# Performance work log

Measured on AMD Instinct MI355X. Metric: run time of the kernel, lower is better.

## Reference

```python
import jax, jax.numpy as jnp
import numpy as np
from jax import lax

B, CIN, HC, D, H, W = 4, 16, 16, 31, 128, 128


def setup_inputs() -> dict:
    key = jax.random.key(0)
    k1, k2, k3, k4, k5 = jax.random.split(key, 5)
    inputs = jax.random.normal(k1, (B, CIN, D, H, W), dtype=jnp.float32)
    # Conv3d weight: [out=2*HC, in=CIN, 3,3,3]
    conv_w = jax.random.normal(k2, (2 * HC, CIN, 3, 3, 3), dtype=jnp.float32) * 0.05
    # FFN weights stored as [in, out] (equivalent to torch Linear weight.T)
    w1 = jax.random.normal(k3, (HC, 2 * HC), dtype=jnp.float32) * 0.1
    w2 = jax.random.normal(k4, (2 * HC, HC), dtype=jnp.float32) * 0.1
    w3 = jax.random.normal(k5, (HC, 2 * HC), dtype=jnp.float32) * 0.1
    return {"inputs": inputs, "conv_w": conv_w, "w1": w1, "w2": w2, "w3": w3,
            "reverse": 0}


def reference(inputs, conv_w, w1, w2, w3, reverse):
    hc = conv_w.shape[0] // 2
    # 3D conv producing 2*hc gate channels  [B, 2hc, D, H, W]
    gates = lax.conv_general_dilated(
        inputs, conv_w, window_strides=(1, 1, 1), padding='SAME',
        dimension_numbers=('NCDHW', 'OIDHW', 'NCDHW'))
    Z = jnp.tanh(gates[:, :hc])            # [B, hc, D, H, W]
    F = jax.nn.sigmoid(gates[:, hc:])
    # scan over depth (spectral) dim; h0 = 0 reproduces h = (1-f)*z at step 0
    Zs = jnp.moveaxis(Z, 2, 0)             # [D, B, hc, H, W]
    Fs = jnp.moveaxis(F, 2, 0)
    if reverse:
        Zs, Fs = Zs[::-1], Fs[::-1]

    def step(h, zf):
        z, f = zf
        h = f * h + (1.0 - f) * z
        return h, h

    h0 = jnp.zeros_like(Zs[0])
    _, hs = lax.scan(step, h0, (Zs, Fs))   # [D, B, hc, H, W]
    if reverse:
        hs = hs[::-1]
    out = jnp.moveaxis(hs, 0, 2)           # [B, hc, D, H, W]
    # channel-enhanced FFN on channel-last layout
    x = jnp.moveaxis(out, 1, -1)           # [B, D, H, W, hc]
    x1 = jnp.dot(jax.nn.gelu(jnp.dot(x, w1), approximate=False), w2)
    g = jnp.dot(x, w3)                     # [B, D, H, W, 2hc]
    a, wg = jnp.split(g, 2, axis=-1)
    y = x1 + a * jax.nn.sigmoid(wg)
    return jnp.moveaxis(y, -1, 1)          # [B, hc, D, H, W]
```

## Files before the change

kernel.cpp:

```cpp
#include <hip/hip_runtime.h>
#include <hip/hip_fp16.h>

#define HC 16
#define CIN 16
#define BD 31
#define HH 128
#define WW 128
#define PLANE (HH*WW)
#define CH_STRIDE (BD*PLANE)

typedef __attribute__((ext_vector_type(8))) short bf16x8;
typedef __attribute__((ext_vector_type(16))) float f32x16;

__device__ __forceinline__ float sigmoid_fast(float x) {
    return __builtin_amdgcn_rcpf(1.0f + __expf(-x));
}
__device__ __forceinline__ float tanh_fast(float x) {
    return fmaf(2.0f, __builtin_amdgcn_rcpf(1.0f + __expf(-2.0f * x)), -1.0f);
}
__device__ __forceinline__ ushort f2bf(float f) {
    unsigned u = __float_as_uint(f);
    u = (u + 0x7fffu + ((u >> 16) & 1u)) >> 16;
    return (ushort)u;
}
__device__ __forceinline__ unsigned pack_bf2(float lo, float hi) {
    unsigned r;
    asm("v_cvt_pk_bf16_f32 %0, %1, %2" : "=v"(r) : "v"(lo), "v"(hi));
    return r;
}
__device__ __forceinline__ float gelu_as(float s) {
    float z  = 0.70710678118f * s;
    float az = fabsf(z);
    float t  = __builtin_amdgcn_rcpf(fmaf(0.3275911f, az, 1.0f));
    float p  = t * (0.254829592f + t * (-0.284496736f + t * (1.421413741f
             + t * (-1.453152027f + t * 1.061405429f))));
    float e  = __expf(-z * z);
    float er = copysignf(1.0f - p * e, z);
    return 0.5f * s * (1.0f + er);
}

__global__ void wprep_all(const float* __restrict__ cw,
                          const float* __restrict__ w1,
                          const float* __restrict__ w2,
                          const float* __restrict__ w3,
                          ushort* __restrict__ wtab,
                          ushort* __restrict__ wtab2)
{
    int idx = blockIdx.x * 256 + threadIdx.x;
    if (idx < 13824) {
        int j    = idx & 7;
        int lane = (idx >> 3) & 63;
        int t    = (idx >> 9) % 9;
        int kd   = (idx >> 9) / 9;
        int co = lane & 31;
        int ci = 8 * (lane >> 5) + j;
        int kh = t / 3, kw = t % 3;
        wtab[idx] = f2bf(cw[(co * CIN + ci) * 27 + kd * 9 + kh * 3 + kw]);
        return;
    }
    idx -= 13824;
    if (idx >= 2048) return;
    int e    = idx & 7;
    int lane = (idx >> 3) & 63;
    int tbl  = idx >> 9;
    int m  = lane & 31;
    int hi = lane >> 5;
    int k  = (e & 3) + 8 * (e >> 2) + 4 * hi;
    float v = 0.f;
    if (tbl == 0)      v = w1[k * 32 + m];
    else if (tbl == 3) v = w3[k * 32 + m];
    else {
        int mf = tbl - 1;
        if (m < 16) v = w2[(k + 16 * mf) * 16 + m];
    }
    wtab2[idx] = f2bf(v);
}

__global__ __launch_bounds__(256)
void xprep_kernel(const float* __restrict__ inp, char* __restrict__ xT)
{
    __shared__ float tile[16][256];
    int t  = threadIdx.x;
    int hp = blockIdx.x & 63;
    int g  = blockIdx.x >> 6;
    int d  = g % BD;
    int b  = g / BD;

    size_t src = (size_t)b * CIN * CH_STRIDE + (size_t)d * PLANE + hp * 256;
    #pragma unroll
    for (int c = 0; c < 16; ++c)
        tile[c][t] = inp[src + (size_t)c * CH_STRIDE + t];
    __syncthreads();

    int w  = t & 127;
    int rr = t >> 7;
    char* rowp = xT + (((size_t)(b * BD + d) * 128) + hp * 2 + rr) * 4096;
    #pragma unroll
    for (int q = 0; q < 2; ++q) {
        uint4 pk;
        pk.x = (unsigned)f2bf(tile[q*8+0][t]) | ((unsigned)f2bf(tile[q*8+1][t]) << 16);
        pk.y = (unsigned)f2bf(tile[q*8+2][t]) | ((unsigned)f2bf(tile[q*8+3][t]) << 16);
        pk.z = (unsigned)f2bf(tile[q*8+4][t]) | ((unsigned)f2bf(tile[q*8+5][t]) << 16);
        pk.w = (unsigned)f2bf(tile[q*8+6][t]) | ((unsigned)f2bf(tile[q*8+7][t]) << 16);
        unsigned off = ((unsigned)((w + 1) * 32 + q * 16) ^ (((unsigned)(w + 1) & 0xE) << 3)) - 32;
        *(uint4*)(rowp + off) = pk;
    }
}

#define SLOT_B (3 * 4224)

__device__ __forceinline__ void gload_lds16(const void* g, void* l) {
    __builtin_amdgcn_global_load_lds(
        (const __attribute__((address_space(1))) unsigned int*)g,
        (__attribute__((address_space(3))) unsigned int*)l, 16, 0, 0);
}

__global__ __launch_bounds__(256, 2)
void qrnn_fused(const char* __restrict__ xT,
                const ushort* __restrict__ wtab,
                const ushort* __restrict__ wtab2,
                float* __restrict__ out,
                const int* __restrict__ rev_p)
{
    __shared__ __align__(16) char slab[4][SLOT_B];

    int p = blockIdx.x;
    int logical = (p & 7) * 64 + (p >> 3);
    int b  = logical >> 7;
    int ht = logical & 127;
    int rev = rev_p[0];

    int lane = threadIdx.x & 63;
    int wid  = threadIdx.x >> 6;
    int wl   = lane & 31;
    int hi   = lane >> 5;
    int cio  = hi * 16;

    const bf16x8* wt = (const bf16x8*)wtab;
    bf16x8 af[27];
    #pragma unroll
    for (int t = 0; t < 27; ++t) af[t] = wt[t * 64 + lane];

    const bf16x8* W2 = (const bf16x8*)wtab2;
    bf16x8 af1  = W2[lane];
    bf16x8 af2a = W2[64 + lane];
    bf16x8 af2b = W2[128 + lane];
    bf16x8 af3  = W2[192 + lane];

    unsigned bpo[3];
    #pragma unroll
    for (int dwn = 0; dwn < 3; ++dwn) {
        unsigned wc = (unsigned)(wl + dwn);
        bpo[dwn] = (unsigned)(wid * 1024) + ((wc * 32 + cio) ^ ((wc & 0xE) << 3));
    }

    for (int i = threadIdx.x; i < 4 * 3 * 32; i += 256) {
        int s = i / 96;
        int r = (i / 32) % 3;
        int k = i & 31;
        int off = (k < 8) ? (k * 4) : (4128 + (k - 8) * 4);
        *(int*)(slab[s] + r * 4224 + off) = 0;
    }

    auto zero_slot = [&](int s) {
        for (int i = threadIdx.x; i < 768; i += 256) {
            int r = i >> 8;
            int k = i & 255;
            *(uint4*)(slab[s] + r * 4224 + 32 + k * 16) = uint4{0, 0, 0, 0};
        }
    };

    auto stage = [&](int s, int plane) {
        const char* pl = xT + ((size_t)(b * BD + plane) * 128) * 4096;
        for (int c = wid; c < 12; c += 4) {
            int rr = c >> 2, ch = c & 3;
            int h = ht - 1 + rr;
            char* dst = slab[s] + rr * 4224 + 32 + ch * 1024;
            if ((unsigned)h < (unsigned)HH)
                gload_lds16(pl + (size_t)h * 4096 + ch * 1024 + lane * 16, dst);
            else
                *(uint4*)(dst + lane * 16) = uint4{0, 0, 0, 0};
        }
    };

    f32x16 zacc;
    #pragma unroll
    for (int r = 0; r < 16; ++r) zacc[r] = 0.f;

    auto convd = [&](int d) -> f32x16 {
        f32x16 A = zacc;
        #pragma unroll
        for (int kd = 0; kd < 3; ++kd) {
            const char* sb = slab[(d - 1 + kd) & 3];
            #pragma unroll
            for (int t = 0; t < 9; ++t) {
                bf16x8 bfr = *(const bf16x8*)(sb + (t / 3) * 4224 + bpo[t % 3]);
                A = __builtin_amdgcn_mfma_f32_32x32x16_bf16(af[kd * 9 + t], bfr, A, 0, 0, 0);
            }
        }
        return A;
    };

    float h[8];
    #pragma unroll
    for (int j = 0; j < 8; ++j) h[j] = 0.f;

    float* obase = out + (size_t)b * HC * CH_STRIDE + ht * WW + wid * 32 + wl;

    auto tail = [&](const f32x16& A, int d) {
        union { bf16x8 v; unsigned u[4]; } bx;
        #pragma unroll
        for (int r = 0; r < 8; ++r) {
            float z = tanh_fast(A[r]);
            float f = sigmoid_fast(A[r + 8]);
            h[r] = z + f * (h[r] - z);
        }
        #pragma unroll
        for (int q = 0; q < 4; ++q)
            bx.u[q] = pack_bf2(h[2 * q], h[2 * q + 1]);

        f32x16 a1 = __builtin_amdgcn_mfma_f32_32x32x16_bf16(af1, bx.v, zacc, 0, 0, 0);
        f32x16 a3 = __builtin_amdgcn_mfma_f32_32x32x16_bf16(af3, bx.v, zacc, 0, 0, 0);

        union { bf16x8 v; unsigned u[4]; } b2a, b2b;
        #pragma unroll
        for (int q = 0; q < 4; ++q) {
            b2a.u[q] = pack_bf2(gelu_as(a1[2 * q]),     gelu_as(a1[2 * q + 1]));
            b2b.u[q] = pack_bf2(gelu_as(a1[8 + 2 * q]), gelu_as(a1[8 + 2 * q + 1]));
        }
        f32x16 a2 = __builtin_amdgcn_mfma_f32_32x32x16_bf16(af2a, b2a.v, zacc, 0, 0, 0);
        a2 = __builtin_amdgcn_mfma_f32_32x32x16_bf16(af2b, b2b.v, a2, 0, 0, 0);

        float* ob = obase + (size_t)d * PLANE;
        #pragma unroll
        for (int r = 0; r < 8; ++r) {
            int c = (r & 3) + 8 * (r >> 2) + 4 * hi;
            ob[(size_t)c * CH_STRIDE] = a2[r] + a3[r] * sigmoid_fast(a3[r + 8]);
        }
    };

    int d0  = rev ? (BD - 1) : 0;
    int sgn = rev ? -1 : 1;
    int oobq = rev ? -1 : BD;

    stage(d0 & 3, d0);
    stage((d0 + sgn) & 3, d0 + sgn);
    zero_slot((d0 - sgn) & 3);
    __syncthreads();

    f32x16 accP;
    {
        int q = d0 + 2 * sgn;
        if (q >= 0 && q < BD) stage(q & 3, q);
        accP = convd(d0);
        __syncthreads();
    }

    #pragma unroll 1
    for (int i = 1; i < BD; ++i) {
        int d = d0 + sgn * i;
        int q = d + 2 * sgn;
        if (q >= 0 && q < BD) stage(q & 3, q);
        else if (q == oobq)   zero_slot(q & 3);

        f32x16 acc = convd(d);
        tail(accP, d - sgn);
        accP = acc;

        __syncthreads();
    }
    tail(accP, d0 + sgn * (BD - 1));
}

extern "C" void kernel_launch(void* const* d_in, const int* in_sizes, int n_in,
                              void* d_out, int out_size, void* d_ws, size_t ws_size,
                              hipStream_t stream)
{
    const float* inp = (const float*)d_in[0];
    const float* cw  = (const float*)d_in[1];
    const float* w1  = (const float*)d_in[2];
    const float* w2  = (const float*)d_in[3];
    const float* w3  = (const float*)d_in[4];
    const int*   rev = (const int*)d_in[5];

    ushort* wtab  = (ushort*)d_ws;
    ushort* wtab2 = (ushort*)((char*)d_ws + 27648);
    char*   xT    = (char*)d_ws + 32768;

    wprep_all<<<dim3(62), dim3(256), 0, stream>>>(cw, w1, w2, w3, wtab, wtab2);

    xprep_kernel<<<dim3(7936), dim3(256), 0, stream>>>(inp, xT);

    qrnn_fused<<<dim3(512), dim3(256), 0, stream>>>(
        xT, wtab, wtab2, (float*)d_out, rev);
}
```

Before: 143.0 us.

## Split FFN out of scan kernel into separate MFMA kernel; merge weight prep into xprep

Moves the channel FFN (GELU MLP plus gated branch) out of the serial conv+scan kernel into a new fully parallel MFMA kernel. The scan kernel now writes the bf16 hidden state to a workspace buffer. Weight preparation is folded into the xprep launch as extra blocks, which removes one kernel launch. The aim is to shorten the serial per-depth critical path and cut register pressure in the scan kernel. The cost is an extra round trip through global memory for the hidden state, about 32 MB written and read back, and one more launch. Folding weight prep into xprep assumes the weight tables are ready by the time the scan kernel runs, which stream ordering provides.

```diff
diff --git a/kernel.cpp b/kernel.cpp
--- a/kernel.cpp
+++ b/kernel.cpp
@@ -39,46 +39,46 @@
     return 0.5f * s * (1.0f + er);
 }
 
-__global__ void wprep_all(const float* __restrict__ cw,
-                          const float* __restrict__ w1,
-                          const float* __restrict__ w2,
-                          const float* __restrict__ w3,
-                          ushort* __restrict__ wtab,
-                          ushort* __restrict__ wtab2)
+__global__ __launch_bounds__(256)
+void xprep_kernel(const float* __restrict__ inp, char* __restrict__ xT,
+                  const float* __restrict__ cw,
+                  const float* __restrict__ w1,
+                  const float* __restrict__ w2,
+                  const float* __restrict__ w3,
+                  ushort* __restrict__ wtab, ushort* __restrict__ wtab2)
 {
-    int idx = blockIdx.x * 256 + threadIdx.x;
-    if (idx < 13824) {
-        int j    = idx & 7;
+    if (blockIdx.x >= 7936) {
+        int idx = (blockIdx.x - 7936) * 256 + threadIdx.x;
+        if (idx < 13824) {
+            int j    = idx & 7;
+            int lane = (idx >> 3) & 63;
+            int t    = (idx >> 9) % 9;
+            int kd   = (idx >> 9) / 9;
+            int co = lane & 31;
+            int ci = 8 * (lane >> 5) + j;
+            int kh = t / 3, kw = t % 3;
+            wtab[idx] = f2bf(cw[(co * CIN + ci) * 27 + kd * 9 + kh * 3 + kw]);
+            return;
+        }
+        idx -= 13824;
+        if (idx >= 2048) return;
+        int e    = idx & 7;
         int lane = (idx >> 3) & 63;
-        int t    = (idx >> 9) % 9;
-        int kd   = (idx >> 9) / 9;
-        int co = lane & 31;
-        int ci = 8 * (lane >> 5) + j;
-        int kh = t / 3, kw = t % 3;
-        wtab[idx] = f2bf(cw[(co * CIN + ci) * 27 + kd * 9 + kh * 3 + kw]);
+        int tbl  = idx >> 9;
+        int m  = lane & 31;
+        int hi = lane >> 5;
+        int k  = (e & 3) + 8 * (e >> 2) + 4 * hi;
+        float v = 0.f;
+        if (tbl == 0)      v = w1[k * 32 + m];
+        else if (tbl == 3) v = w3[k * 32 + m];
+        else {
+            int mf = tbl - 1;
+            if (m < 16) v = w2[(k + 16 * mf) * 16 + m];
+        }
+        wtab2[idx] = f2bf(v);
         return;
     }
-    idx -= 13824;
-    if (idx >= 2048) return;
-    int e    = idx & 7;
-    int lane = (idx >> 3) & 63;
-    int tbl  = idx >> 9;
-    int m  = lane & 31;
-    int hi = lane >> 5;
-    int k  = (e & 3) + 8 * (e >> 2) + 4 * hi;
-    float v = 0.f;
-    if (tbl == 0)      v = w1[k * 32 + m];
-    else if (tbl == 3) v = w3[k * 32 + m];
-    else {
-        int mf = tbl - 1;
-        if (m < 16) v = w2[(k + 16 * mf) * 16 + m];
-    }
-    wtab2[idx] = f2bf(v);
-}
-
-__global__ __launch_bounds__(256)
-void xprep_kernel(const float* __restrict__ inp, char* __restrict__ xT)
-{
+
     __shared__ float tile[16][256];
     int t  = threadIdx.x;
     int hp = blockIdx.x & 63;
@@ -116,11 +116,10 @@
 }
 
 __global__ __launch_bounds__(256, 2)
-void qrnn_fused(const char* __restrict__ xT,
-                const ushort* __restrict__ wtab,
-                const ushort* __restrict__ wtab2,
-                float* __restrict__ out,
-                const int* __restrict__ rev_p)
+void qrnn_convscan(const char* __restrict__ xT,
+                   const ushort* __restrict__ wtab,
+                   char* __restrict__ hbuf,
+                   const int* __restrict__ rev_p)
 {
     __shared__ __align__(16) char slab[4][SLOT_B];
 
@@ -140,12 +139,6 @@
     bf16x8 af[27];
     #pragma unroll
     for (int t = 0; t < 27; ++t) af[t] = wt[t * 64 + lane];
-
-    const bf16x8* W2 = (const bf16x8*)wtab2;
-    bf16x8 af1  = W2[lane];
-    bf16x8 af2a = W2[64 + lane];
-    bf16x8 af2b = W2[128 + lane];
-    bf16x8 af3  = W2[192 + lane];
 
     unsigned bpo[3];
     #pragma unroll
@@ -205,10 +198,11 @@
     #pragma unroll
     for (int j = 0; j < 8; ++j) h[j] = 0.f;
 
-    float* obase = out + (size_t)b * HC * CH_STRIDE + ht * WW + wid * 32 + wl;
+    int pix = ht * WW + wid * 32 + wl;
+    char* hb0 = hbuf + ((size_t)b * BD * PLANE + pix) * 32 + hi * 16;
 
     auto tail = [&](const f32x16& A, int d) {
-        union { bf16x8 v; unsigned u[4]; } bx;
+        union { uint4 u4; unsigned u[4]; } bx;
         #pragma unroll
         for (int r = 0; r < 8; ++r) {
             float z = tanh_fast(A[r]);
@@ -218,25 +212,7 @@
         #pragma unroll
         for (int q = 0; q < 4; ++q)
             bx.u[q] = pack_bf2(h[2 * q], h[2 * q + 1]);
-
-        f32x16 a1 = __builtin_amdgcn_mfma_f32_32x32x16_bf16(af1, bx.v, zacc, 0, 0, 0);
-        f32x16 a3 = __builtin_amdgcn_mfma_f32_32x32x16_bf16(af3, bx.v, zacc, 0, 0, 0);
-
-        union { bf16x8 v; unsigned u[4]; } b2a, b2b;
-        #pragma unroll
-        for (int q = 0; q < 4; ++q) {
-            b2a.u[q] = pack_bf2(gelu_as(a1[2 * q]),     gelu_as(a1[2 * q + 1]));
-            b2b.u[q] = pack_bf2(gelu_as(a1[8 + 2 * q]), gelu_as(a1[8 + 2 * q + 1]));
-        }
-        f32x16 a2 = __builtin_amdgcn_mfma_f32_32x32x16_bf16(af2a, b2a.v, zacc, 0, 0, 0);
-        a2 = __builtin_amdgcn_mfma_f32_32x32x16_bf16(af2b, b2b.v, a2, 0, 0, 0);
-
-        float* ob = obase + (size_t)d * PLANE;
-        #pragma unroll
-        for (int r = 0; r < 8; ++r) {
-            int c = (r & 3) + 8 * (r >> 2) + 4 * hi;
-            ob[(size_t)c * CH_STRIDE] = a2[r] + a3[r] * sigmoid_fast(a3[r + 8]);
-        }
+        *(uint4*)(hb0 + (size_t)d * (PLANE * 32)) = bx.u4;
     };
 
     int d0  = rev ? (BD - 1) : 0;
@@ -270,6 +246,57 @@
         __syncthreads();
     }
     tail(accP, d0 + sgn * (BD - 1));
+}
+
+__global__ __launch_bounds__(256)
+void mlp_mfma_kernel(const char* __restrict__ hbuf,
+                     const ushort* __restrict__ wtab2,
+                     float* __restrict__ out)
+{
+    int lane = threadIdx.x & 63;
+    int wid  = threadIdx.x >> 6;
+    int p    = lane & 31;
+    int hi   = lane >> 5;
+
+    size_t tile = (size_t)blockIdx.x * 4 + wid;
+    size_t ptg  = tile * 32 + p;
+
+    const bf16x8* W = (const bf16x8*)wtab2;
+    bf16x8 af1  = W[lane];
+    bf16x8 af2a = W[64 + lane];
+    bf16x8 af2b = W[128 + lane];
+    bf16x8 af3  = W[192 + lane];
+    bf16x8 bx   = *(const bf16x8*)(hbuf + ptg * 32 + hi * 16);
+
+    f32x16 zacc;
+    #pragma unroll
+    for (int r = 0; r < 16; ++r) zacc[r] = 0.f;
+
+    f32x16 a1 = __builtin_amdgcn_mfma_f32_32x32x16_bf16(af1, bx, zacc, 0, 0, 0);
+    f32x16 a3 = __builtin_amdgcn_mfma_f32_32x32x16_bf16(af3, bx, zacc, 0, 0, 0);
+
+    union { bf16x8 v; unsigned u[4]; } b2a, b2b;
+    #pragma unroll
+    for (int q = 0; q < 4; ++q) {
+        b2a.u[q] = pack_bf2(gelu_as(a1[2 * q]),     gelu_as(a1[2 * q + 1]));
+        b2b.u[q] = pack_bf2(gelu_as(a1[8 + 2 * q]), gelu_as(a1[8 + 2 * q + 1]));
+    }
+
+    f32x16 a2 = __builtin_amdgcn_mfma_f32_32x32x16_bf16(af2a, b2a.v, zacc, 0, 0, 0);
+    a2 = __builtin_amdgcn_mfma_f32_32x32x16_bf16(af2b, b2b.v, a2, 0, 0, 0);
+
+    int bd  = (int)(ptg >> 14);
+    int pix = (int)(ptg & 16383);
+    int b   = bd / BD;
+    int d   = bd % BD;
+    float* obase = out + (size_t)b * HC * CH_STRIDE + (size_t)d * PLANE + pix;
+
+    #pragma unroll
+    for (int r = 0; r < 8; ++r) {
+        int c = (r & 3) + 8 * (r >> 2) + 4 * hi;
+        float y = a2[r] + a3[r] * sigmoid_fast(a3[r + 8]);
+        obase[(size_t)c * CH_STRIDE] = y;
+    }
 }
 
 extern "C" void kernel_launch(void* const* d_in, const int* in_sizes, int n_in,
@@ -286,11 +313,14 @@
     ushort* wtab  = (ushort*)d_ws;
     ushort* wtab2 = (ushort*)((char*)d_ws + 27648);
     char*   xT    = (char*)d_ws + 32768;
-
-    wprep_all<<<dim3(62), dim3(256), 0, stream>>>(cw, w1, w2, w3, wtab, wtab2);
-
-    xprep_kernel<<<dim3(7936), dim3(256), 0, stream>>>(inp, xT);
-
-    qrnn_fused<<<dim3(512), dim3(256), 0, stream>>>(
-        xT, wtab, wtab2, (float*)d_out, rev);
-}
+    char*   hbuf  = (char*)d_ws + 32768 + (size_t)4 * BD * 128 * 4096;
+
+    xprep_kernel<<<dim3(7998), dim3(256), 0, stream>>>(
+        inp, xT, cw, w1, w2, w3, wtab, wtab2);
+
+    qrnn_convscan<<<dim3(512), dim3(256), 0, stream>>>(
+        xT, wtab, hbuf, rev);
+
+    mlp_mfma_kernel<<<dim3(15872), dim3(256), 0, stream>>>(
+        hbuf, wtab2, (float*)d_out);
+}
```

New measurement: 149.3 us. +4.4%, slower.
